# Kernel optimization log

Hardware: AMD Instinct MI355X
Metric: run time of the kernel (lower is better)

## Reference

```python
import jax, jax.numpy as jnp
import numpy as np

# 2^22-point radix-2 DIT FFT; NOTE the original code applies tf.abs at EVERY
# recursion level (not just the top), so each butterfly stage is followed by a
# magnitude + recomplexification. We reproduce that exact (non-standard) math.
N = 1 << 22
STAGES = 22


def _bitrev_perm(n, bits):
    # vectorized bit-reversal permutation (the order induced by the even/odd
    # decimation inputs[0::2] / inputs[1::2] recursion)
    x = np.arange(n)
    r = np.zeros(n, dtype=np.int64)
    for b in range(bits):
        r = (r << 1) | ((x >> b) & 1)
    return r


_PERM = jnp.asarray(_bitrev_perm(N, STAGES))


def setup_inputs() -> dict:
    key = jax.random.key(0)
    x = jax.random.normal(key, (N,), dtype=jnp.float32)
    return {"x": x}


def reference(x):
    # base case of the recursion: length-1 leaves are the bit-reversed inputs
    y = x[_PERM].astype(jnp.complex64)
    for s in range(1, STAGES + 1):  # fixed log2(N) stages, not a data loop
        m = 1 << s                  # sub-FFT size at this stage
        yb = y.reshape(N // m, m)   # [num_blocks, m]
        e = yb[:, : m // 2]         # 'even' sub-results
        o = yb[:, m // 2:]          # 'odd'  sub-results
        # twiddles W(m, k) = exp(-2*pi*i*k/m)
        tw = jnp.exp(
            jnp.complex64(-2j * np.pi) * jnp.arange(m // 2, dtype=jnp.float32) / m
        ).astype(jnp.complex64)
        t = tw[None, :] * o
        # butterfly then tf.abs (applied at every level in the original)
        mag = jnp.abs(jnp.concatenate([e + t, e - t], axis=1)).reshape(N)
        y = mag.astype(jnp.complex64) if s < STAGES else mag
    return y  # float32 magnitudes, shape [N]
```

## Files before the change

kernel.cpp:

```cpp
#include <hip/hip_runtime.h>
#include <math.h>


#define NBITS 22
#define RSQ2 0.70710678118654752440f

__device__ __forceinline__ float hsqrt(float x) { return __builtin_amdgcn_sqrtf(x); }

__device__ __forceinline__ void bf(float& e, float& o, float c, float s) {
    float rp = fmaf(c, o, e);
    float rm = fmaf(-c, o, e);
    float im = s * o;
    float im2 = im * im;
    e = hsqrt(fmaf(rp, rp, im2));
    o = hsqrt(fmaf(rm, rm, im2));
}
__device__ __forceinline__ void bf0(float& e, float& o) {
    float a = e + o, b = e - o;
    e = fabsf(a); o = fabsf(b);
}
__device__ __forceinline__ void bfq(float& e, float& o) {
    float h = hsqrt(fmaf(e, e, o * o));
    e = h; o = h;
}

__device__ __constant__ float KC[16] = {
    1.f, 0.980785280f, 0.923879533f, 0.831469612f, 0.707106781f, 0.555570233f,
    0.382683432f, 0.195090322f, 0.f, -0.195090322f, -0.382683432f, -0.555570233f,
    -0.707106781f, -0.831469612f, -0.923879533f, -0.980785280f };
__device__ __constant__ float KS[16] = {
    0.f, 0.195090322f, 0.382683432f, 0.555570233f, 0.707106781f, 0.831469612f,
    0.923879533f, 0.980785280f, 1.f, 0.980785280f, 0.923879533f, 0.831469612f,
    0.707106781f, 0.555570233f, 0.382683432f, 0.195090322f };

template <int L>
__device__ __forceinline__ void radixN(float* v, float c, float s) {
    float ca[L], sa[L];
    ca[L - 1] = c; sa[L - 1] = s;
#pragma unroll
    for (int a = L - 1; a > 0; --a) {
        ca[a - 1] = fmaf(-2.f * sa[a], sa[a], 1.f);
        sa[a - 1] = 2.f * sa[a] * ca[a];
    }
#pragma unroll
    for (int a = 0; a < L; ++a) {
        const int half = 1 << a;
#pragma unroll
        for (int d = 0; d < half; ++d) {
            const int k = d << (4 - a);
            float cd = fmaf(ca[a], KC[k], -sa[a] * KS[k]);
            float sd = fmaf(sa[a], KC[k],  ca[a] * KS[k]);
#pragma unroll
            for (int g = d; g < (1 << L); g += 2 * half)
                bf(v[g], v[g + half], cd, sd);
        }
    }
}

__device__ __forceinline__ void radix8z(float v[8]) {
    bf0(v[0], v[1]); bf0(v[2], v[3]); bf0(v[4], v[5]); bf0(v[6], v[7]);
    bf0(v[0], v[2]); bf0(v[4], v[6]);
    bfq(v[1], v[3]); bfq(v[5], v[7]);
    bf0(v[0], v[4]);
    bf(v[1], v[5], RSQ2, RSQ2);
    bfq(v[2], v[6]);
    bf(v[3], v[7], -RSQ2, RSQ2);
}

__global__ __launch_bounds__(256, 8) void fft_perm(const float* __restrict__ x,
                                                   float* __restrict__ y) {
    __shared__ float lds[64 * 65];
    const unsigned tid = threadIdx.x;
    const unsigned tx = tid & 63, g = tid >> 6;
    const unsigned C0 = (blockIdx.x & 31) * 64;
    const unsigned B0 = (blockIdx.x >> 5) * 64;

#pragma unroll
    for (int k = 0; k < 16; ++k) {
        unsigned r = g * 16 + k;
        unsigned a = __brev(C0 + r) >> (32 - 11);
        lds[r * 65 + tx] = x[a * 2048u + B0 + tx];
    }
    __syncthreads();

    float v[8];
#pragma unroll
    for (int q = 0; q < 2; ++q) {
        unsigned task = tid + 256u * q;
        unsigned c = task >> 3, grp = task & 7;
#pragma unroll
        for (int j = 0; j < 8; ++j) v[j] = lds[(grp * 8 + j) * 65 + c];
        radix8z(v);
        unsigned pr = __brev(B0 + c) >> (32 - 11);
        float* dst = y + pr * 2048u + C0 + grp * 8;
        *(float4*)(dst)     = make_float4(v[0], v[1], v[2], v[3]);
        *(float4*)(dst + 4) = make_float4(v[4], v[5], v[6], v[7]);
    }
}

__global__ __launch_bounds__(256, 4) void fft_low(float* __restrict__ y) {
    __shared__ float lds[8448];
    const unsigned t = threadIdx.x;
    const unsigned base = blockIdx.x * 8192;
    const unsigned lo = t & 7, hi = t >> 3;
    float v[32];

    {
        const float* src = y + base + lo + 256u * hi;
#pragma unroll
        for (int j = 0; j < 32; ++j) v[j] = src[8 * j];
        float r = (float)lo * (1.f / 256.f);
        radixN<5>(v, __builtin_amdgcn_cosf(r), __builtin_amdgcn_sinf(r));
#pragma unroll
        for (int j = 0; j < 32; ++j) {
            unsigned q = lo + 8u * j + 256u * hi;
            lds[q + (q >> 5)] = v[j];
        }
    }
    __syncthreads();

    {
#pragma unroll
        for (int j = 0; j < 32; ++j) {
            unsigned q = t + 256u * j;
            v[j] = lds[q + (q >> 5)];
        }
        float r = (float)t * (1.f / 8192.f);
        radixN<5>(v, __builtin_amdgcn_cosf(r), __builtin_amdgcn_sinf(r));
        float* dst = y + base + t;
#pragma unroll
        for (int j = 0; j < 32; ++j) dst[256u * j] = v[j];
    }
}

__global__ __launch_bounds__(256, 4) void fft_high(float* __restrict__ y) {
    __shared__ float lds[512 * 17 + 32];
    const unsigned tt = threadIdx.x;
    const unsigned li = tt & 15, u5 = tt >> 4;
    const unsigned low = blockIdx.x * 16 + li;
    float v[32];

    {
        const float* src = y + low;
#pragma unroll
        for (int j = 0; j < 32; ++j) v[j] = src[8192u * (32u * u5 + j)];
        float r = (float)low * (1.f / 262144.f);
        radixN<5>(v, __builtin_amdgcn_cosf(r), __builtin_amdgcn_sinf(r));
#pragma unroll
        for (int j = 0; j < 32; ++j) {
            unsigned trow = 32u * u5 + j;
            lds[trow * 17 + (trow >> 5) + li] = v[j];
        }
    }
    __syncthreads();

#pragma unroll
    for (int b = 0; b < 2; ++b) {
        const unsigned t0 = 2u * u5 + b;
        float* w = v + 16 * b;
#pragma unroll
        for (int j = 0; j < 16; ++j) {
            unsigned trow = t0 + 32u * j;
            w[j] = lds[trow * 17 + (trow >> 5) + li];
        }
        float r = ((float)low + 8192.f * (float)t0) * (1.f / 4194304.f);
        radixN<4>(w, __builtin_amdgcn_cosf(r), __builtin_amdgcn_sinf(r));
#pragma unroll
        for (int j = 0; j < 16; ++j)
            y[low + 8192u * (t0 + 32u * j)] = w[j];
    }
}

extern "C" void kernel_launch(void* const* d_in, const int* in_sizes, int n_in,
                              void* d_out, int out_size, void* d_ws, size_t ws_size,
                              hipStream_t stream) {
    const float* x = (const float*)d_in[0];
    float* out = (float*)d_out;

    fft_perm<<<dim3(1024), dim3(256), 0, stream>>>(x, out);
    fft_low<<<dim3(512), dim3(256), 0, stream>>>(out);
    fft_high<<<dim3(512), dim3(256), 0, stream>>>(out);
}
```

Baseline: 100.7 us.

## Stage global loads/stores through LDS with float4 coalescing and staggered ordering

fft_low and fft_high now read their whole tile into padded LDS with float4 global loads before computing. fft_high also writes results back through LDS using float4 stores. fft_perm switches to float4 global reads, and both per-block loops rotate their starting index by blockIdx to spread accesses across memory channels. This targets poorly coalesced strided scalar global accesses, especially the 8192-stride columns in fft_high. In exchange it uses more LDS, adds another barrier, and lowers occupancy hints (launch bounds 4→2 for fft_low/fft_high and 8→4 for fft_perm).

```diff
diff --git a/kernel.cpp b/kernel.cpp
--- a/kernel.cpp
+++ b/kernel.cpp
@@ -67,19 +67,26 @@
     bf(v[3], v[7], -RSQ2, RSQ2);
 }
 
-__global__ __launch_bounds__(256, 8) void fft_perm(const float* __restrict__ x,
+__device__ __forceinline__ unsigned apad(unsigned q) { return q + 4u * (q >> 8); }
+__device__ __forceinline__ unsigned bpad(unsigned t, unsigned li) {
+    return 20u * t + li + 8u * (t >> 5);
+}
+
+__global__ __launch_bounds__(256, 4) void fft_perm(const float* __restrict__ x,
                                                    float* __restrict__ y) {
     __shared__ float lds[64 * 65];
     const unsigned tid = threadIdx.x;
-    const unsigned tx = tid & 63, g = tid >> 6;
     const unsigned C0 = (blockIdx.x & 31) * 64;
     const unsigned B0 = (blockIdx.x >> 5) * 64;
-
-#pragma unroll
-    for (int k = 0; k < 16; ++k) {
-        unsigned r = g * 16 + k;
+    const unsigned qi = tid & 15, rr = tid >> 4;
+
+#pragma unroll
+    for (int k = 0; k < 4; ++k) {
+        unsigned r = rr + 16u * k;
         unsigned a = __brev(C0 + r) >> (32 - 11);
-        lds[r * 65 + tx] = x[a * 2048u + B0 + tx];
+        float4 f = *(const float4*)(x + a * 2048u + B0 + 4u * qi);
+        float* p = &lds[r * 65u + 4u * qi];
+        p[0] = f.x; p[1] = f.y; p[2] = f.z; p[3] = f.w;
     }
     __syncthreads();
 
@@ -89,68 +96,81 @@
         unsigned task = tid + 256u * q;
         unsigned c = task >> 3, grp = task & 7;
 #pragma unroll
-        for (int j = 0; j < 8; ++j) v[j] = lds[(grp * 8 + j) * 65 + c];
+        for (int j = 0; j < 8; ++j) v[j] = lds[(grp * 8u + j) * 65u + c];
         radix8z(v);
         unsigned pr = __brev(B0 + c) >> (32 - 11);
-        float* dst = y + pr * 2048u + C0 + grp * 8;
+        float* dst = y + pr * 2048u + C0 + grp * 8u;
         *(float4*)(dst)     = make_float4(v[0], v[1], v[2], v[3]);
         *(float4*)(dst + 4) = make_float4(v[4], v[5], v[6], v[7]);
     }
 }
 
-__global__ __launch_bounds__(256, 4) void fft_low(float* __restrict__ y) {
-    __shared__ float lds[8448];
+__global__ __launch_bounds__(256, 2) void fft_low(float* __restrict__ y) {
+    __shared__ float lds[8316];
     const unsigned t = threadIdx.x;
-    const unsigned base = blockIdx.x * 8192;
+    const unsigned base = blockIdx.x * 8192u;
+    float v[32];
+
+    {
+        const float4* __restrict__ src4 = (const float4*)(y + base);
+#pragma unroll
+        for (int k = 0; k < 8; ++k) {
+            unsigned kk = ((unsigned)k + blockIdx.x) & 7u;
+            float4 f = src4[t + 256u * kk];
+            *(float4*)&lds[apad(4u * (t + 256u * kk))] = f;
+        }
+    }
+    __syncthreads();
+
     const unsigned lo = t & 7, hi = t >> 3;
-    float v[32];
-
-    {
-        const float* src = y + base + lo + 256u * hi;
-#pragma unroll
-        for (int j = 0; j < 32; ++j) v[j] = src[8 * j];
+    {
+#pragma unroll
+        for (int j = 0; j < 32; ++j) v[j] = lds[apad(lo + 8u * j + 256u * hi)];
         float r = (float)lo * (1.f / 256.f);
         radixN<5>(v, __builtin_amdgcn_cosf(r), __builtin_amdgcn_sinf(r));
 #pragma unroll
-        for (int j = 0; j < 32; ++j) {
-            unsigned q = lo + 8u * j + 256u * hi;
-            lds[q + (q >> 5)] = v[j];
-        }
-    }
-    __syncthreads();
-
-    {
-#pragma unroll
-        for (int j = 0; j < 32; ++j) {
-            unsigned q = t + 256u * j;
-            v[j] = lds[q + (q >> 5)];
-        }
+        for (int j = 0; j < 32; ++j) lds[apad(lo + 8u * j + 256u * hi)] = v[j];
+    }
+    __syncthreads();
+
+    {
+#pragma unroll
+        for (int j = 0; j < 32; ++j) v[j] = lds[apad(t + 256u * j)];
         float r = (float)t * (1.f / 8192.f);
         radixN<5>(v, __builtin_amdgcn_cosf(r), __builtin_amdgcn_sinf(r));
         float* dst = y + base + t;
 #pragma unroll
-        for (int j = 0; j < 32; ++j) dst[256u * j] = v[j];
-    }
-}
-
-__global__ __launch_bounds__(256, 4) void fft_high(float* __restrict__ y) {
-    __shared__ float lds[512 * 17 + 32];
+        for (int j = 0; j < 32; ++j) {
+            unsigned jj = ((unsigned)j + blockIdx.x) & 31u;
+            dst[256u * jj] = v[jj];
+        }
+    }
+}
+
+__global__ __launch_bounds__(256, 2) void fft_high(float* __restrict__ y) {
+    __shared__ float lds[10356];
     const unsigned tt = threadIdx.x;
+    const unsigned low0 = blockIdx.x * 16u;
+    float4* __restrict__ Y4 = (float4*)y;
+    const unsigned lq = tt & 3, tv = tt >> 2;
+    float v[32];
+
+#pragma unroll
+    for (int k = 0; k < 8; ++k) {
+        unsigned t = tv + 64u * (((unsigned)k + blockIdx.x) & 7u);
+        float4 f = Y4[(low0 >> 2) + lq + 2048u * t];
+        *(float4*)&lds[bpad(t, 4u * lq)] = f;
+    }
+    __syncthreads();
+
     const unsigned li = tt & 15, u5 = tt >> 4;
-    const unsigned low = blockIdx.x * 16 + li;
-    float v[32];
-
-    {
-        const float* src = y + low;
-#pragma unroll
-        for (int j = 0; j < 32; ++j) v[j] = src[8192u * (32u * u5 + j)];
-        float r = (float)low * (1.f / 262144.f);
+    {
+#pragma unroll
+        for (int j = 0; j < 32; ++j) v[j] = lds[bpad(32u * u5 + j, li)];
+        float r = (float)(low0 + li) * (1.f / 262144.f);
         radixN<5>(v, __builtin_amdgcn_cosf(r), __builtin_amdgcn_sinf(r));
 #pragma unroll
-        for (int j = 0; j < 32; ++j) {
-            unsigned trow = 32u * u5 + j;
-            lds[trow * 17 + (trow >> 5) + li] = v[j];
-        }
+        for (int j = 0; j < 32; ++j) lds[bpad(32u * u5 + j, li)] = v[j];
     }
     __syncthreads();
 
@@ -159,15 +179,18 @@
         const unsigned t0 = 2u * u5 + b;
         float* w = v + 16 * b;
 #pragma unroll
-        for (int j = 0; j < 16; ++j) {
-            unsigned trow = t0 + 32u * j;
-            w[j] = lds[trow * 17 + (trow >> 5) + li];
-        }
-        float r = ((float)low + 8192.f * (float)t0) * (1.f / 4194304.f);
+        for (int j = 0; j < 16; ++j) w[j] = lds[bpad(t0 + 32u * j, li)];
+        float r = ((float)(low0 + li) + 8192.f * (float)t0) * (1.f / 4194304.f);
         radixN<4>(w, __builtin_amdgcn_cosf(r), __builtin_amdgcn_sinf(r));
 #pragma unroll
-        for (int j = 0; j < 16; ++j)
-            y[low + 8192u * (t0 + 32u * j)] = w[j];
+        for (int j = 0; j < 16; ++j) lds[bpad(t0 + 32u * j, li)] = w[j];
+    }
+    __syncthreads();
+
+#pragma unroll
+    for (int k = 0; k < 8; ++k) {
+        unsigned t = tv + 64u * (((unsigned)k + 5u + blockIdx.x) & 7u);
+        Y4[(low0 >> 2) + lq + 2048u * t] = *(float4*)&lds[bpad(t, 4u * lq)];
     }
 }
 
```

New measurement: 103.1 us. +2.3%, slower.
